# Optimization experiments

Hardware: AMD Instinct MI355X
Metric: run time of the kernel (lower is better)

## Reference

```python
import jax, jax.numpy as jnp
import numpy as np

B, C, H, W = 16, 15, 256, 256

def setup_inputs() -> dict:
    key = jax.random.key(0)
    k1, k2, k3 = jax.random.split(key, 3)
    output = jax.random.normal(k1, (B, C, H, W), dtype=jnp.float32)
    label0 = jax.random.normal(k2, (B, C, H, W), dtype=jnp.float32)
    label1 = jax.random.uniform(k3, (B, C, H, W), dtype=jnp.float32)
    return {"output": output, "label0": label0, "label1": label1}

def reference(output, label0, label1):
    # Fused masked-L1 reduction over the whole tensor (replaces per-(b,c) loop)
    loss = jnp.sum(jnp.abs(output - label0) * label1)
    nonzero_num = jnp.sum(label0 != 0)  # total count of nonzero target entries
    # if nonzero_num == 0: loss -> 0, denom -> 1
    safe_denom = jnp.where(nonzero_num == 0, 1, nonzero_num).astype(loss.dtype)
    loss = jnp.where(nonzero_num == 0, jnp.zeros_like(loss), loss)
    return loss / safe_denom
```

## Files before the change

kernel.cpp:

```cpp
#include <hip/hip_runtime.h>


#define REDUCE_THREADS 256
#define S1_BLOCKS 1920

struct Partial {
    float s;
    unsigned int c;
};

__device__ __forceinline__ void accum4(const float4& o, const float4& a,
                                       const float4& w, float& sum,
                                       unsigned int& cnt) {
    sum += fabsf(o.x - a.x) * w.x;
    sum += fabsf(o.y - a.y) * w.y;
    sum += fabsf(o.z - a.z) * w.z;
    sum += fabsf(o.w - a.w) * w.w;
    cnt += (a.x != 0.0f) + (a.y != 0.0f) + (a.z != 0.0f) + (a.w != 0.0f);
}

template <bool EXACT2>
__global__ __launch_bounds__(REDUCE_THREADS)
void depth_loss_stage1(const float4* __restrict__ out,
                       const float4* __restrict__ l0,
                       const float4* __restrict__ l1,
                       Partial* __restrict__ partials,
                       int n4) {
    const int stride = gridDim.x * REDUCE_THREADS;
    int i = blockIdx.x * REDUCE_THREADS + threadIdx.x;

    float sum = 0.0f;
    unsigned int cnt = 0;

    if constexpr (EXACT2) {
        for (; i < n4; i += 2 * stride) {
            float4 o0 = out[i];
            float4 a0 = l0[i];
            float4 w0 = l1[i];
            float4 o1 = out[i + stride];
            float4 a1 = l0[i + stride];
            float4 w1 = l1[i + stride];
            accum4(o0, a0, w0, sum, cnt);
            accum4(o1, a1, w1, sum, cnt);
        }
    } else {
        for (; i < n4; i += stride) {
            float4 o0 = out[i];
            float4 a0 = l0[i];
            float4 w0 = l1[i];
            accum4(o0, a0, w0, sum, cnt);
        }
    }

    #pragma unroll
    for (int off = 32; off > 0; off >>= 1) {
        sum += __shfl_down(sum, off, 64);
        cnt += __shfl_down(cnt, off, 64);
    }

    __shared__ float        sv[REDUCE_THREADS / 64];
    __shared__ unsigned int sc[REDUCE_THREADS / 64];
    int lane = threadIdx.x & 63;
    int wid  = threadIdx.x >> 6;
    if (lane == 0) { sv[wid] = sum; sc[wid] = cnt; }
    __syncthreads();

    if (threadIdx.x == 0) {
        float bs = 0.0f;
        unsigned int bc = 0;
        #pragma unroll
        for (int i2 = 0; i2 < REDUCE_THREADS / 64; ++i2) { bs += sv[i2]; bc += sc[i2]; }
        Partial p; p.s = bs; p.c = bc;
        partials[blockIdx.x] = p;
    }
}

__global__ __launch_bounds__(REDUCE_THREADS)
void depth_loss_stage2(const Partial* __restrict__ partials,
                       int nblocks,
                       float* __restrict__ out) {
    double sum = 0.0;
    unsigned int cnt = 0;
    for (int i = threadIdx.x; i < nblocks; i += REDUCE_THREADS) {
        Partial p = partials[i];
        sum += (double)p.s;
        cnt += p.c;
    }

    #pragma unroll
    for (int off = 32; off > 0; off >>= 1) {
        sum += __shfl_down(sum, off, 64);
        cnt += __shfl_down(cnt, off, 64);
    }

    __shared__ double       sv[REDUCE_THREADS / 64];
    __shared__ unsigned int sc[REDUCE_THREADS / 64];
    int lane = threadIdx.x & 63;
    int wid  = threadIdx.x >> 6;
    if (lane == 0) { sv[wid] = sum; sc[wid] = cnt; }
    __syncthreads();

    if (threadIdx.x == 0) {
        double bs = 0.0;
        unsigned int bc = 0;
        #pragma unroll
        for (int i = 0; i < REDUCE_THREADS / 64; ++i) { bs += sv[i]; bc += sc[i]; }
        out[0] = (bc == 0) ? 0.0f : (float)(bs / (double)bc);
    }
}

extern "C" void kernel_launch(void* const* d_in, const int* in_sizes, int n_in,
                              void* d_out, int out_size, void* d_ws, size_t ws_size,
                              hipStream_t stream) {
    const float* output = (const float*)d_in[0];
    const float* label0 = (const float*)d_in[1];
    const float* label1 = (const float*)d_in[2];
    int n = in_sizes[0];
    int n4 = n >> 2;

    Partial* partials = (Partial*)d_ws;

    if ((n4 % (S1_BLOCKS * REDUCE_THREADS * 2)) == 0) {
        depth_loss_stage1<true><<<S1_BLOCKS, REDUCE_THREADS, 0, stream>>>(
            (const float4*)output, (const float4*)label0, (const float4*)label1,
            partials, n4);
    } else {
        depth_loss_stage1<false><<<S1_BLOCKS, REDUCE_THREADS, 0, stream>>>(
            (const float4*)output, (const float4*)label0, (const float4*)label1,
            partials, n4);
    }

    depth_loss_stage2<<<1, REDUCE_THREADS, 0, stream>>>(
        partials, S1_BLOCKS, (float*)d_out);
}
```

Baseline: 190.9 us.

## Issue all per-thread vector loads upfront with single-pass grid sized to input

Replaces the grid-stride loop with a single pass where each thread issues 18 dwordx4 loads via inline asm before one vmcnt wait, then accumulates. Grid is sized so the exact input size is covered in one pass. This raises memory-level parallelism to hide latency, at the cost of more registers and a path specialized to an exact element count.

```diff
diff --git a/kernel.cpp b/kernel.cpp
--- a/kernel.cpp
+++ b/kernel.cpp
@@ -2,52 +2,63 @@
 
 
 #define REDUCE_THREADS 256
-#define S1_BLOCKS 1920
+#define EPT 6
+#define S1_BLOCKS 2560
+
+typedef float f32x4 __attribute__((ext_vector_type(4)));
 
 struct Partial {
     float s;
     unsigned int c;
 };
 
-__device__ __forceinline__ void accum4(const float4& o, const float4& a,
-                                       const float4& w, float& sum,
-                                       unsigned int& cnt) {
-    sum += fabsf(o.x - a.x) * w.x;
-    sum += fabsf(o.y - a.y) * w.y;
-    sum += fabsf(o.z - a.z) * w.z;
-    sum += fabsf(o.w - a.w) * w.w;
-    cnt += (a.x != 0.0f) + (a.y != 0.0f) + (a.z != 0.0f) + (a.w != 0.0f);
+__device__ __forceinline__ f32x4 gload4(const f32x4* p) {
+    f32x4 r;
+    asm volatile("global_load_dwordx4 %0, %1, off" : "=v"(r) : "v"(p));
+    return r;
 }
 
-template <bool EXACT2>
+__device__ __forceinline__ void accum4(const f32x4& o, const f32x4& a,
+                                       const f32x4& w, float& sum,
+                                       unsigned int& cnt) {
+    sum += fabsf(o[0] - a[0]) * w[0];
+    sum += fabsf(o[1] - a[1]) * w[1];
+    sum += fabsf(o[2] - a[2]) * w[2];
+    sum += fabsf(o[3] - a[3]) * w[3];
+    cnt += (a[0] != 0.0f) + (a[1] != 0.0f) + (a[2] != 0.0f) + (a[3] != 0.0f);
+}
+
+template <bool EXACT>
 __global__ __launch_bounds__(REDUCE_THREADS)
-void depth_loss_stage1(const float4* __restrict__ out,
-                       const float4* __restrict__ l0,
-                       const float4* __restrict__ l1,
+void depth_loss_stage1(const f32x4* __restrict__ out,
+                       const f32x4* __restrict__ l0,
+                       const f32x4* __restrict__ l1,
                        Partial* __restrict__ partials,
                        int n4) {
-    const int stride = gridDim.x * REDUCE_THREADS;
-    int i = blockIdx.x * REDUCE_THREADS + threadIdx.x;
-
     float sum = 0.0f;
     unsigned int cnt = 0;
 
-    if constexpr (EXACT2) {
-        for (; i < n4; i += 2 * stride) {
-            float4 o0 = out[i];
-            float4 a0 = l0[i];
-            float4 w0 = l1[i];
-            float4 o1 = out[i + stride];
-            float4 a1 = l0[i + stride];
-            float4 w1 = l1[i + stride];
-            accum4(o0, a0, w0, sum, cnt);
-            accum4(o1, a1, w1, sum, cnt);
+    if constexpr (EXACT) {
+        const int base = blockIdx.x * (REDUCE_THREADS * EPT) + threadIdx.x;
+
+        f32x4 o[EPT], a[EPT], w[EPT];
+        #pragma unroll
+        for (int k = 0; k < EPT; ++k) {
+            const int i = base + k * REDUCE_THREADS;
+            o[k] = gload4(&out[i]);
+            a[k] = gload4(&l0[i]);
+            w[k] = gload4(&l1[i]);
         }
+        asm volatile("s_waitcnt vmcnt(0)" ::: "memory");
+        __builtin_amdgcn_sched_barrier(0);
+
+        #pragma unroll
+        for (int k = 0; k < EPT; ++k) accum4(o[k], a[k], w[k], sum, cnt);
     } else {
-        for (; i < n4; i += stride) {
-            float4 o0 = out[i];
-            float4 a0 = l0[i];
-            float4 w0 = l1[i];
+        const int stride = gridDim.x * REDUCE_THREADS;
+        for (int i = blockIdx.x * REDUCE_THREADS + threadIdx.x; i < n4;
+             i += stride) {
+            f32x4 o0 = out[i], a0 = l0[i], w0 = l1[i];
             accum4(o0, a0, w0, sum, cnt);
         }
     }
@@ -120,16 +131,18 @@
 
     Partial* partials = (Partial*)d_ws;
 
-    if ((n4 % (S1_BLOCKS * REDUCE_THREADS * 2)) == 0) {
+    if (n4 == S1_BLOCKS * REDUCE_THREADS * EPT) {
         depth_loss_stage1<true><<<S1_BLOCKS, REDUCE_THREADS, 0, stream>>>(
-            (const float4*)output, (const float4*)label0, (const float4*)label1,
+            (const f32x4*)output, (const f32x4*)label0, (const f32x4*)label1,
             partials, n4);
+        depth_loss_stage2<<<1, REDUCE_THREADS, 0, stream>>>(
+            partials, S1_BLOCKS, (float*)d_out);
     } else {
-        depth_loss_stage1<false><<<S1_BLOCKS, REDUCE_THREADS, 0, stream>>>(
-            (const float4*)output, (const float4*)label0, (const float4*)label1,
+        int blocks = 2048;
+        depth_loss_stage1<false><<<blocks, REDUCE_THREADS, 0, stream>>>(
+            (const f32x4*)output, (const f32x4*)label0, (const f32x4*)label1,
             partials, n4);
+        depth_loss_stage2<<<1, REDUCE_THREADS, 0, stream>>>(
+            partials, blocks, (float*)d_out);
     }
-
-    depth_loss_stage2<<<1, REDUCE_THREADS, 0, stream>>>(
-        partials, S1_BLOCKS, (float*)d_out);
 }
```

Measured after the change: 189.8 us. About the same (-0.6%).
